# Performance work log

Hardware: AMD Instinct MI355X
Metric: run time of the kernel (lower is better)

Reference implementation:

```python
import jax, jax.numpy as jnp
import numpy as np
import math

DIM = 256

def setup_inputs() -> dict:
    key = jax.random.key(0)
    kx, kq, kk, kv = jax.random.split(key, 4)
    B, N, D = 2, 8192, DIM
    x = jax.random.normal(kx, (B, N, D), dtype=jnp.float32)
    s = 1.0 / math.sqrt(D)  # ~ PyTorch Linear init scale
    Wq = jax.random.uniform(kq, (D, D), dtype=jnp.float32, minval=-s, maxval=s)
    Wk = jax.random.uniform(kk, (D, D), dtype=jnp.float32, minval=-s, maxval=s)
    Wv = jax.random.uniform(kv, (D, D), dtype=jnp.float32, minval=-s, maxval=s)
    return {"x": x, "Wq": Wq, "Wk": Wk, "Wv": Wv}

def reference(x, Wq, Wk, Wv):
    # x: [B, N, D]; torch Linear computes x @ W.T
    Q = jnp.einsum('bnd,ed->bne', x, Wq)
    K = jnp.einsum('bnd,ed->bne', x, Wk)
    V = jnp.einsum('bnd,ed->bne', x, Wv)
    D = x.shape[-1]
    scores = jnp.einsum('bqd,bkd->bqk', Q, K) / jnp.sqrt(jnp.float32(D))
    # NOTE: softmax over dim=1 (the query axis), matching the original code
    attn = jax.nn.softmax(scores, axis=1)  # [B, N, N]
    out = jnp.einsum('bqk,bkd->bqd', attn, V)
    return out
```

## Files before the change

kernel.cpp:

```cpp
#include <hip/hip_runtime.h>
#include <hip/hip_bf16.h>


#define N_ 8192
#define SCALE 0.0625f

typedef __attribute__((ext_vector_type(8))) short short8;
typedef __attribute__((ext_vector_type(4))) float f32x4;
typedef __attribute__((ext_vector_type(4))) unsigned short ushort4_t;

__device__ inline unsigned short f2bf(float f) {
    unsigned int x = __float_as_uint(f);
    unsigned int r = (x + 0x7fffu + ((x >> 16) & 1u)) >> 16;
    return (unsigned short)r;
}

__device__ inline short8 ldg8(const unsigned short* p) {
    return *reinterpret_cast<const short8*>(p);
}

__device__ inline short8 cvt8(const float* p) {
    float4 a = *(const float4*)p;
    float4 b = *(const float4*)(p + 4);
    short8 r;
    r[0] = (short)f2bf(a.x); r[1] = (short)f2bf(a.y);
    r[2] = (short)f2bf(a.z); r[3] = (short)f2bf(a.w);
    r[4] = (short)f2bf(b.x); r[5] = (short)f2bf(b.y);
    r[6] = (short)f2bf(b.z); r[7] = (short)f2bf(b.w);
    return r;
}

__device__ inline f32x4 mfma16(short8 a, short8 b, f32x4 c) {
    return __builtin_amdgcn_mfma_f32_16x16x32_bf16(a, b, c, 0, 0, 0);
}

__device__ inline float bf2f(unsigned short u) {
    return __uint_as_float(((unsigned)u) << 16);
}

#define PIN8(v) asm volatile("" : "+v"(v))

typedef __attribute__((address_space(3))) unsigned int lds_u32;
typedef __attribute__((address_space(1))) const unsigned int glb_u32;
__device__ __forceinline__ void gll16(const void* g, void* l) {
    __builtin_amdgcn_global_load_lds((glb_u32*)g, (lds_u32*)l, 16, 0, 0);
}
#define WAIT_VM0()   asm volatile("s_waitcnt vmcnt(0)" ::: "memory")
#define WAIT_LGKM0() asm volatile("s_waitcnt lgkmcnt(0)" ::: "memory")
#define BARRIER()    __builtin_amdgcn_s_barrier()

__global__ __launch_bounds__(256) void k_cvtw(
    const float* __restrict__ Wq, const float* __restrict__ Wk,
    const float* __restrict__ Wv, unsigned short* __restrict__ Wb)
{
    int t = blockIdx.x * 256 + threadIdx.x;
    int e8 = t * 8;
    const float* src = (e8 < 65536) ? Wq + e8
                     : (e8 < 131072) ? Wk + (e8 - 65536)
                                     : Wv + (e8 - 131072);
    *reinterpret_cast<short8*>(Wb + e8) = cvt8(src);
}

__global__ __launch_bounds__(512) void k_proj(
    const float* __restrict__ x, const unsigned short* __restrict__ Wb,
    unsigned short* __restrict__ Qb, unsigned short* __restrict__ Kb,
    unsigned short* __restrict__ Vt)
{
    __shared__ unsigned short sX[64 * 256];
    int rb = blockIdx.x;
    int tid = threadIdx.x, w = tid >> 6, lane = tid & 63;
    int lr = lane & 15, lg = lane >> 4;

#pragma unroll
    for (int i = 0; i < 4; ++i) {
        int g = tid + i * 512;
        int r = g >> 5, c = g & 31;
        int off = (r * 512 + c * 16) ^ ((r & 7) << 4);
        *reinterpret_cast<short8*>(reinterpret_cast<char*>(sX) + off) =
            cvt8(x + (size_t)(rb * 64 + r) * 256 + c * 8);
    }
    __syncthreads();

    f32x4 acc[4][6] = {};
#pragma unroll
    for (int ks = 0; ks < 8; ++ks) {
        int coff = (ks * 32 + lg * 8) * 2;
        short8 xf[4];
#pragma unroll
        for (int rf = 0; rf < 4; ++rf) {
            int row = rf * 16 + lr;
            int off = (row * 512 + coff) ^ ((row & 7) << 4);
            xf[rf] = *reinterpret_cast<const short8*>(
                reinterpret_cast<const char*>(sX) + off);
        }
#pragma unroll
        for (int cf = 0; cf < 6; ++cf) {
            int e = w * 96 + cf * 16 + lr;
            short8 bfr = ldg8(Wb + (size_t)e * 256 + ks * 32 + lg * 8);
#pragma unroll
            for (int rf = 0; rf < 4; ++rf)
                acc[rf][cf] = mfma16(xf[rf], bfr, acc[rf][cf]);
        }
    }

#pragma unroll
    for (int rf = 0; rf < 4; ++rf)
#pragma unroll
        for (int cf = 0; cf < 6; ++cf) {
            int e0c = w * 96 + cf * 16;
            int mat = e0c >> 8;
            int ecol = (e0c & 255) + lr;
            int rbase = rb * 64 + rf * 16 + lg * 4;
            if (mat < 2) {
                unsigned short* dst = (mat == 0) ? Qb : Kb;
#pragma unroll
                for (int r = 0; r < 4; ++r)
                    dst[(size_t)(rbase + r) * 256 + ecol] = f2bf(acc[rf][cf][r]);
            } else {
                int bidx = rbase >> 13, nr = rbase & 8191;
                ushort4_t v;
#pragma unroll
                for (int r = 0; r < 4; ++r) v[r] = f2bf(acc[rf][cf][r]);
                *reinterpret_cast<ushort4_t*>(
                    Vt + ((size_t)bidx * 256 + ecol) * 8192 + nr) = v;
            }
        }
}

__global__ __launch_bounds__(512, 1) void k_zv(
    const unsigned short* __restrict__ Qb, const unsigned short* __restrict__ Kb,
    unsigned short* __restrict__ Vt)
{
    extern __shared__ char smem[];
    __shared__ float zred[8][32];
    __shared__ float zfin[64];
    const int kt = blockIdx.x, b = blockIdx.y;
    const int tid = threadIdx.x, w = tid >> 6, lane = tid & 63;
    const int lr = lane & 15, lg = lane >> 4;
    const int qs = w & 3, kh = w >> 2;

    short8 kfr[2][8];
#pragma unroll
    for (int kn = 0; kn < 2; ++kn)
#pragma unroll
        for (int ks = 0; ks < 8; ++ks) {
            kfr[kn][ks] = ldg8(
                Kb + (size_t)(b * N_ + kt * 64 + kh * 32 + kn * 16 + lr) * 256
                   + ks * 32 + lg * 8);
            PIN8(kfr[kn][ks]);
        }

    int eoff[8], doff[8];
#pragma unroll
    for (int i = 0; i < 8; ++i) {
        int L = i * 512 + w * 64 + lane;
        int r = L >> 5, c = (L & 31) ^ (r & 7);
        eoff[i] = r * 256 + c * 8;
        doff[i] = L * 16;
    }
    const unsigned short* qbase = Qb + (size_t)b * N_ * 256;

#pragma unroll
    for (int i = 0; i < 8; ++i)
        gll16(qbase + eoff[i], smem + doff[i]);

    float zs0 = 0.f, zs1 = 0.f;
    for (int it = 0; it < 64; ++it) {
        const int cur = it & 1;
        const char* sQ = smem + cur * 65536;

        WAIT_VM0();
        BARRIER();
        __builtin_amdgcn_sched_barrier(0);

        if (it + 1 < 64) {
            const unsigned short* qsrc = qbase + (size_t)(it + 1) * 128 * 256;
            char* nQ = smem + (cur ^ 1) * 65536;
#pragma unroll
            for (int i = 0; i < 8; ++i)
                gll16(qsrc + eoff[i], nQ + doff[i]);
        }

        f32x4 acc[2][2] = {};
        __builtin_amdgcn_s_setprio(1);
#pragma unroll
        for (int ks = 0; ks < 8; ++ks) {
            int coff = (ks * 32 + lg * 8) * 2;
#pragma unroll
            for (int qf = 0; qf < 2; ++qf) {
                int row = qs * 32 + qf * 16 + lr;
                int off = (row * 512 + coff) ^ ((row & 7) << 4);
                short8 qa = *reinterpret_cast<const short8*>(sQ + off);
                acc[qf][0] = mfma16(qa, kfr[0][ks], acc[qf][0]);
                acc[qf][1] = mfma16(qa, kfr[1][ks], acc[qf][1]);
            }
        }
        __builtin_amdgcn_s_setprio(0);

#pragma unroll
        for (int qf = 0; qf < 2; ++qf)
#pragma unroll
            for (int r = 0; r < 4; ++r) {
                zs0 += __expf(acc[qf][0][r] * SCALE);
                zs1 += __expf(acc[qf][1][r] * SCALE);
            }
    }

    zs0 += __shfl_xor(zs0, 16); zs0 += __shfl_xor(zs0, 32);
    zs1 += __shfl_xor(zs1, 16); zs1 += __shfl_xor(zs1, 32);
    if (lg == 0) {
        zred[w][lr]      = zs0;
        zred[w][16 + lr] = zs1;
    }
    __syncthreads();
    if (tid < 64) {
        int kh2 = tid >> 5, kc = tid & 31;
        float z = zred[kh2 * 4 + 0][kc] + zred[kh2 * 4 + 1][kc] +
                  zred[kh2 * 4 + 2][kc] + zred[kh2 * 4 + 3][kc];
        zfin[tid] = 1.0f / z;
    }
    __syncthreads();

#pragma unroll
    for (int i = 0; i < 4; ++i) {
        int G = i * 512 + tid;
        int d = G >> 3, c = G & 7;
        unsigned short* p =
            Vt + ((size_t)b * 256 + d) * 8192 + kt * 64 + c * 8;
        short8 v = *reinterpret_cast<short8*>(p);
        short8 o;
#pragma unroll
        for (int j = 0; j < 8; ++j)
            o[j] = (short)f2bf(bf2f((unsigned short)v[j]) * zfin[c * 8 + j]);
        *reinterpret_cast<short8*>(p) = o;
    }
}

__global__ __launch_bounds__(512, 1) void k_attn(
    const unsigned short* __restrict__ Qb, const unsigned short* __restrict__ Kb,
    const unsigned short* __restrict__ Vt, float* __restrict__ out)
{
    extern __shared__ char smem[];
    const int qt = blockIdx.x, b = blockIdx.y;
    const int tid = threadIdx.x, w = tid >> 6, lane = tid & 63;
    const int lr = lane & 15, lg = lane >> 4;
    const int qbase = qt * 64;
    const int wqs = w >> 2;
    const int wks = w & 3;
    const int wds = w & 3;
    const int q0 = wqs * 32;

    const unsigned short* srcK[4];
    const unsigned short* srcV[4];
#pragma unroll
    for (int i = 0; i < 4; ++i) {
        int L = w * 256 + i * 64 + lane;
        int r = L >> 5, c = (L & 31) ^ (r & 7);
        srcK[i] = Kb + (size_t)(b * N_ + r) * 256 + c * 8;
        int d = L >> 3, c2 = (L & 7) ^ (d & 7);
        srcV[i] = Vt + ((size_t)b * 256 + d) * 8192 + c2 * 8;
    }

#pragma unroll
    for (int i = 0; i < 4; ++i) {
        gll16(srcK[i], smem + (size_t)(w * 256 + i * 64) * 16);
        gll16(srcV[i], smem + 65536 + (size_t)(w * 256 + i * 64) * 16);
        srcK[i] += 64 * 256;
        srcV[i] += 64;
    }

    short8 qfr[2][8];
#pragma unroll
    for (int qf = 0; qf < 2; ++qf) {
        const unsigned short* qrow =
            Qb + (size_t)(b * N_ + qbase + q0 + qf * 16 + lr) * 256;
#pragma unroll
        for (int ks = 0; ks < 8; ++ks) {
            qfr[qf][ks] = ldg8(qrow + ks * 32 + lg * 8);
            PIN8(qfr[qf][ks]);
        }
    }

    f32x4 acco[2][4] = {};

    for (int kt = 0; kt < 128; ++kt) {
        const int cur = kt & 1;
        char* sK = smem + cur * 32768;
        char* sV = smem + 65536 + cur * 32768;
        char* sP = smem + 131072;

        WAIT_VM0();
        BARRIER();
        __builtin_amdgcn_sched_barrier(0);

        if (kt + 1 < 128) {
            char* nK = smem + (cur ^ 1) * 32768;
            char* nV = smem + 65536 + (cur ^ 1) * 32768;
#pragma unroll
            for (int i = 0; i < 4; ++i) {
                gll16(srcK[i], nK + (size_t)(w * 256 + i * 64) * 16);
                gll16(srcV[i], nV + (size_t)(w * 256 + i * 64) * 16);
                srcK[i] += 64 * 256;
                srcV[i] += 64;
            }
        }

        f32x4 sacc[2] = {};
        __builtin_amdgcn_s_setprio(1);
#pragma unroll
        for (int ks = 0; ks < 8; ++ks) {
            int krow = wks * 16 + lr;
            int coff = (ks * 32 + lg * 8) * 2;
            int off = (krow * 512 + coff) ^ ((krow & 7) << 4);
            short8 kb = *reinterpret_cast<const short8*>(sK + off);
            sacc[0] = mfma16(qfr[0][ks], kb, sacc[0]);
            sacc[1] = mfma16(qfr[1][ks], kb, sacc[1]);
        }
        __builtin_amdgcn_s_setprio(0);

#pragma unroll
        for (int qf = 0; qf < 2; ++qf)
#pragma unroll
            for (int r = 0; r < 4; ++r) {
                float p = __expf(sacc[qf][r] * SCALE);
                int q = q0 + qf * 16 + lg * 4 + r;
                int kcol = wks * 16 + lr;
                int off = (q * 128 + kcol * 2) ^ ((q & 7) << 4);
                *reinterpret_cast<unsigned short*>(sP + off) = f2bf(p);
            }

        WAIT_LGKM0();
        BARRIER();
        __builtin_amdgcn_sched_barrier(0);

        __builtin_amdgcn_s_setprio(1);
#pragma unroll
        for (int kk = 0; kk < 2; ++kk) {
            int coff = (kk * 32 + lg * 8) * 2;
            short8 pa[2];
#pragma unroll
            for (int qf = 0; qf < 2; ++qf) {
                int qq = q0 + qf * 16 + lr;
                int offa = (qq * 128 + coff) ^ ((qq & 7) << 4);
                pa[qf] = *reinterpret_cast<const short8*>(sP + offa);
            }
#pragma unroll
            for (int df = 0; df < 4; ++df) {
                int d = wds * 64 + df * 16 + lr;
                int offb = (d * 128 + coff) ^ ((d & 7) << 4);
                short8 vb = *reinterpret_cast<const short8*>(sV + offb);
                acco[0][df] = mfma16(pa[0], vb, acco[0][df]);
                acco[1][df] = mfma16(pa[1], vb, acco[1][df]);
            }
        }
        __builtin_amdgcn_s_setprio(0);
    }

#pragma unroll
    for (int qf = 0; qf < 2; ++qf)
#pragma unroll
        for (int df = 0; df < 4; ++df) {
            int d = wds * 64 + df * 16 + lr;
            int q0r = qbase + q0 + qf * 16 + lg * 4;
#pragma unroll
            for (int r = 0; r < 4; ++r)
                out[(size_t)(b * N_ + q0r + r) * 256 + d] = acco[qf][df][r];
        }
}

extern "C" void kernel_launch(void* const* d_in, const int* in_sizes, int n_in,
                              void* d_out, int out_size, void* d_ws, size_t ws_size,
                              hipStream_t stream)
{
    const float* x  = (const float*)d_in[0];
    const float* Wq = (const float*)d_in[1];
    const float* Wk = (const float*)d_in[2];
    const float* Wv = (const float*)d_in[3];

    char* ws = (char*)d_ws;
    unsigned short* Qb = (unsigned short*)(ws);
    unsigned short* Kb = (unsigned short*)(ws + 8388608);
    unsigned short* Vt = (unsigned short*)(ws + 16777216);
    unsigned short* Wb = (unsigned short*)(ws + 25165824);
    float* out = (float*)d_out;

    k_cvtw<<<dim3(96), dim3(256), 0, stream>>>(Wq, Wk, Wv, Wb);
    k_proj<<<dim3(256), dim3(512), 0, stream>>>(x, Wb, Qb, Kb, Vt);

    hipFuncSetAttribute((const void*)k_zv,
                        hipFuncAttributeMaxDynamicSharedMemorySize, 131072);
    k_zv<<<dim3(128, 2), dim3(512), 131072, stream>>>(Qb, Kb, Vt);

    hipFuncSetAttribute((const void*)k_attn,
                        hipFuncAttributeMaxDynamicSharedMemorySize, 139264);
    k_attn<<<dim3(128, 2), dim3(512), 139264, stream>>>(Qb, Kb, Vt, out);
}
```

Baseline: 303.9 us.

## Software-pipeline PV matmul one tile behind QK and load V fragments directly

The attention loop now computes the P·V product for the previous key tile in the same phase as the current Q·K product, with P double-buffered in shared memory so one barrier per iteration is removed. V is no longer staged through LDS; each lane loads its V fragments straight from global memory into registers, which shrinks dynamic shared memory from about 136KB to 80KB. The trade-off is uncached global V loads per wave (redundant across waves sharing d-columns) and possible latency exposure, since the loads are issued right before use, plus a tail epilogue for the last tile.

After: 449.4 us. 1.48x slower.

```diff
diff --git a/kernel.cpp b/kernel.cpp
--- a/kernel.cpp
+++ b/kernel.cpp
@@ -251,23 +251,23 @@
     const int q0 = wqs * 32;
 
     const unsigned short* srcK[4];
-    const unsigned short* srcV[4];
 #pragma unroll
     for (int i = 0; i < 4; ++i) {
         int L = w * 256 + i * 64 + lane;
         int r = L >> 5, c = (L & 31) ^ (r & 7);
         srcK[i] = Kb + (size_t)(b * N_ + r) * 256 + c * 8;
-        int d = L >> 3, c2 = (L & 7) ^ (d & 7);
-        srcV[i] = Vt + ((size_t)b * 256 + d) * 8192 + c2 * 8;
-    }
-
+    }
 #pragma unroll
     for (int i = 0; i < 4; ++i) {
         gll16(srcK[i], smem + (size_t)(w * 256 + i * 64) * 16);
-        gll16(srcV[i], smem + 65536 + (size_t)(w * 256 + i * 64) * 16);
         srcK[i] += 64 * 256;
-        srcV[i] += 64;
-    }
+    }
+
+    const unsigned short* vrow[4];
+#pragma unroll
+    for (int df = 0; df < 4; ++df)
+        vrow[df] = Vt + ((size_t)(b * 256 + wds * 64 + df * 16 + lr)) * 8192
+                      + lg * 8;
 
     short8 qfr[2][8];
 #pragma unroll
@@ -285,23 +285,31 @@
 
     for (int kt = 0; kt < 128; ++kt) {
         const int cur = kt & 1;
-        char* sK = smem + cur * 32768;
-        char* sV = smem + 65536 + cur * 32768;
-        char* sP = smem + 131072;
+        char* sK  = smem + cur * 32768;
+        char* sPw = smem + 65536 + cur * 8192;
+        const char* sPr = smem + 65536 + (cur ^ 1) * 8192;
 
         WAIT_VM0();
+        WAIT_LGKM0();
         BARRIER();
         __builtin_amdgcn_sched_barrier(0);
 
         if (kt + 1 < 128) {
             char* nK = smem + (cur ^ 1) * 32768;
-            char* nV = smem + 65536 + (cur ^ 1) * 32768;
 #pragma unroll
             for (int i = 0; i < 4; ++i) {
                 gll16(srcK[i], nK + (size_t)(w * 256 + i * 64) * 16);
-                gll16(srcV[i], nV + (size_t)(w * 256 + i * 64) * 16);
                 srcK[i] += 64 * 256;
-                srcV[i] += 64;
+            }
+        }
+
+        short8 vfr[8];
+        if (kt > 0) {
+            int kg = (kt - 1) * 64;
+#pragma unroll
+            for (int df = 0; df < 4; ++df) {
+                vfr[df * 2 + 0] = ldg8(vrow[df] + kg);
+                vfr[df * 2 + 1] = ldg8(vrow[df] + kg + 32);
             }
         }
 
@@ -316,6 +324,24 @@
             sacc[0] = mfma16(qfr[0][ks], kb, sacc[0]);
             sacc[1] = mfma16(qfr[1][ks], kb, sacc[1]);
         }
+        if (kt > 0) {
+#pragma unroll
+            for (int kk = 0; kk < 2; ++kk) {
+                int coff = (kk * 32 + lg * 8) * 2;
+                short8 pa[2];
+#pragma unroll
+                for (int qf = 0; qf < 2; ++qf) {
+                    int qq = q0 + qf * 16 + lr;
+                    int offa = (qq * 128 + coff) ^ ((qq & 7) << 4);
+                    pa[qf] = *reinterpret_cast<const short8*>(sPr + offa);
+                }
+#pragma unroll
+                for (int df = 0; df < 4; ++df) {
+                    acco[0][df] = mfma16(pa[0], vfr[df * 2 + kk], acco[0][df]);
+                    acco[1][df] = mfma16(pa[1], vfr[df * 2 + kk], acco[1][df]);
+                }
+            }
+        }
         __builtin_amdgcn_s_setprio(0);
 
 #pragma unroll
@@ -326,14 +352,21 @@
                 int q = q0 + qf * 16 + lg * 4 + r;
                 int kcol = wks * 16 + lr;
                 int off = (q * 128 + kcol * 2) ^ ((q & 7) << 4);
-                *reinterpret_cast<unsigned short*>(sP + off) = f2bf(p);
-            }
-
-        WAIT_LGKM0();
-        BARRIER();
-        __builtin_amdgcn_sched_barrier(0);
-
-        __builtin_amdgcn_s_setprio(1);
+                *reinterpret_cast<unsigned short*>(sPw + off) = f2bf(p);
+            }
+    }
+
+    WAIT_LGKM0();
+    BARRIER();
+    {
+        const char* sPr = smem + 65536 + (127 & 1) * 8192;
+        int kg = 127 * 64;
+        short8 vfr[8];
+#pragma unroll
+        for (int df = 0; df < 4; ++df) {
+            vfr[df * 2 + 0] = ldg8(vrow[df] + kg);
+            vfr[df * 2 + 1] = ldg8(vrow[df] + kg + 32);
+        }
 #pragma unroll
         for (int kk = 0; kk < 2; ++kk) {
             int coff = (kk * 32 + lg * 8) * 2;
@@ -342,18 +375,14 @@
             for (int qf = 0; qf < 2; ++qf) {
                 int qq = q0 + qf * 16 + lr;
                 int offa = (qq * 128 + coff) ^ ((qq & 7) << 4);
-                pa[qf] = *reinterpret_cast<const short8*>(sP + offa);
+                pa[qf] = *reinterpret_cast<const short8*>(sPr + offa);
             }
 #pragma unroll
             for (int df = 0; df < 4; ++df) {
-                int d = wds * 64 + df * 16 + lr;
-                int offb = (d * 128 + coff) ^ ((d & 7) << 4);
-                short8 vb = *reinterpret_cast<const short8*>(sV + offb);
-                acco[0][df] = mfma16(pa[0], vb, acco[0][df]);
-                acco[1][df] = mfma16(pa[1], vb, acco[1][df]);
-            }
-        }
-        __builtin_amdgcn_s_setprio(0);
+                acco[0][df] = mfma16(pa[0], vfr[df * 2 + kk], acco[0][df]);
+                acco[1][df] = mfma16(pa[1], vfr[df * 2 + kk], acco[1][df]);
+            }
+        }
     }
 
 #pragma unroll
@@ -392,6 +421,6 @@
     k_zv<<<dim3(128, 2), dim3(512), 131072, stream>>>(Qb, Kb, Vt);
 
     hipFuncSetAttribute((const void*)k_attn,
-                        hipFuncAttributeMaxDynamicSharedMemorySize, 139264);
-    k_attn<<<dim3(128, 2), dim3(512), 139264, stream>>>(Qb, Kb, Vt, out);
-}
+                        hipFuncAttributeMaxDynamicSharedMemorySize, 81920);
+    k_attn<<<dim3(128, 2), dim3(512), 81920, stream>>>(Qb, Kb, Vt, out);
+}
```

## Software-pipeline QK and PV stages, load V fragments directly to registers

Applied to the files above, without the earlier changes.

Restructures the attention loop so the PV product for tile t-1 runs in the same phase as the QK product for tile t, using double-buffered P in shared memory, which removes one barrier per iteration. V fragments are now loaded straight from global memory into registers, one tile ahead, instead of being staged through LDS. This cuts LDS usage from 139264 to 81920 bytes. The cost is more registers and uncoalesced-ish per-lane global V loads whose latency must hide behind a single iteration.

After: 425.3 us. +39.9%, slower.

```diff
diff --git a/kernel.cpp b/kernel.cpp
--- a/kernel.cpp
+++ b/kernel.cpp
@@ -251,23 +251,23 @@
     const int q0 = wqs * 32;
 
     const unsigned short* srcK[4];
-    const unsigned short* srcV[4];
 #pragma unroll
     for (int i = 0; i < 4; ++i) {
         int L = w * 256 + i * 64 + lane;
         int r = L >> 5, c = (L & 31) ^ (r & 7);
         srcK[i] = Kb + (size_t)(b * N_ + r) * 256 + c * 8;
-        int d = L >> 3, c2 = (L & 7) ^ (d & 7);
-        srcV[i] = Vt + ((size_t)b * 256 + d) * 8192 + c2 * 8;
-    }
-
+    }
 #pragma unroll
     for (int i = 0; i < 4; ++i) {
         gll16(srcK[i], smem + (size_t)(w * 256 + i * 64) * 16);
-        gll16(srcV[i], smem + 65536 + (size_t)(w * 256 + i * 64) * 16);
         srcK[i] += 64 * 256;
-        srcV[i] += 64;
-    }
+    }
+
+    const unsigned short* vrow[4];
+#pragma unroll
+    for (int df = 0; df < 4; ++df)
+        vrow[df] = Vt + ((size_t)(b * 256 + wds * 64 + df * 16 + lr)) * 8192
+                      + lg * 8;
 
     short8 qfr[2][8];
 #pragma unroll
@@ -282,78 +282,105 @@
     }
 
     f32x4 acco[2][4] = {};
-
-    for (int kt = 0; kt < 128; ++kt) {
-        const int cur = kt & 1;
-        char* sK = smem + cur * 32768;
-        char* sV = smem + 65536 + cur * 32768;
-        char* sP = smem + 131072;
-
-        WAIT_VM0();
-        BARRIER();
-        __builtin_amdgcn_sched_barrier(0);
-
-        if (kt + 1 < 128) {
-            char* nK = smem + (cur ^ 1) * 32768;
-            char* nV = smem + 65536 + (cur ^ 1) * 32768;
-#pragma unroll
-            for (int i = 0; i < 4; ++i) {
-                gll16(srcK[i], nK + (size_t)(w * 256 + i * 64) * 16);
-                gll16(srcV[i], nV + (size_t)(w * 256 + i * 64) * 16);
-                srcK[i] += 64 * 256;
-                srcV[i] += 64;
-            }
-        }
-
-        f32x4 sacc[2] = {};
-        __builtin_amdgcn_s_setprio(1);
-#pragma unroll
-        for (int ks = 0; ks < 8; ++ks) {
-            int krow = wks * 16 + lr;
-            int coff = (ks * 32 + lg * 8) * 2;
-            int off = (krow * 512 + coff) ^ ((krow & 7) << 4);
-            short8 kb = *reinterpret_cast<const short8*>(sK + off);
-            sacc[0] = mfma16(qfr[0][ks], kb, sacc[0]);
-            sacc[1] = mfma16(qfr[1][ks], kb, sacc[1]);
-        }
-        __builtin_amdgcn_s_setprio(0);
-
-#pragma unroll
-        for (int qf = 0; qf < 2; ++qf)
-#pragma unroll
-            for (int r = 0; r < 4; ++r) {
-                float p = __expf(sacc[qf][r] * SCALE);
-                int q = q0 + qf * 16 + lg * 4 + r;
-                int kcol = wks * 16 + lr;
-                int off = (q * 128 + kcol * 2) ^ ((q & 7) << 4);
-                *reinterpret_cast<unsigned short*>(sP + off) = f2bf(p);
-            }
-
-        WAIT_LGKM0();
-        BARRIER();
-        __builtin_amdgcn_sched_barrier(0);
-
-        __builtin_amdgcn_s_setprio(1);
+    short8 vfA[8], vfB[8];
+    int kg = 0;
+
+#define AITER(CUR, VLOAD, VCONS, DO_STAGE, DO_PV)                             \
+    do {                                                                      \
+        WAIT_VM0();                                                           \
+        WAIT_LGKM0();                                                         \
+        BARRIER();                                                            \
+        __builtin_amdgcn_sched_barrier(0);                                    \
+        char* sK  = smem + (CUR) * 32768;                                     \
+        char* sPw = smem + 65536 + (CUR) * 8192;                              \
+        const char* sPr = smem + 65536 + ((CUR) ^ 1) * 8192;                  \
+        if (DO_STAGE) {                                                       \
+            char* nK = smem + ((CUR) ^ 1) * 32768;                            \
+            _Pragma("unroll") for (int i = 0; i < 4; ++i) {                   \
+                gll16(srcK[i], nK + (size_t)(w * 256 + i * 64) * 16);         \
+                srcK[i] += 64 * 256;                                          \
+            }                                                                 \
+        }                                                                     \
+        _Pragma("unroll") for (int df = 0; df < 4; ++df) {                    \
+            VLOAD[df * 2 + 0] = ldg8(vrow[df] + kg);                          \
+            VLOAD[df * 2 + 1] = ldg8(vrow[df] + kg + 32);                     \
+        }                                                                     \
+        kg += 64;                                                             \
+        f32x4 sacc[2] = {};                                                   \
+        __builtin_amdgcn_s_setprio(1);                                        \
+        _Pragma("unroll") for (int ks = 0; ks < 8; ++ks) {                    \
+            int krow = wks * 16 + lr;                                         \
+            int coff = (ks * 32 + lg * 8) * 2;                                \
+            int off = (krow * 512 + coff) ^ ((krow & 7) << 4);                \
+            short8 kb = *reinterpret_cast<const short8*>(sK + off);           \
+            sacc[0] = mfma16(qfr[0][ks], kb, sacc[0]);                        \
+            sacc[1] = mfma16(qfr[1][ks], kb, sacc[1]);                        \
+        }                                                                     \
+        if (DO_PV) {                                                          \
+            _Pragma("unroll") for (int kk = 0; kk < 2; ++kk) {                \
+                int coff = (kk * 32 + lg * 8) * 2;                            \
+                short8 pa0, pa1;                                              \
+                {                                                             \
+                    int qq = q0 + lr;                                         \
+                    int offa = (qq * 128 + coff) ^ ((qq & 7) << 4);           \
+                    pa0 = *reinterpret_cast<const short8*>(sPr + offa);       \
+                }                                                             \
+                {                                                             \
+                    int qq = q0 + 16 + lr;                                    \
+                    int offa = (qq * 128 + coff) ^ ((qq & 7) << 4);           \
+                    pa1 = *reinterpret_cast<const short8*>(sPr + offa);       \
+                }                                                             \
+                _Pragma("unroll") for (int df = 0; df < 4; ++df) {            \
+                    acco[0][df] = mfma16(pa0, VCONS[df * 2 + kk], acco[0][df]); \
+                    acco[1][df] = mfma16(pa1, VCONS[df * 2 + kk], acco[1][df]); \
+                }                                                             \
+            }                                                                 \
+        }                                                                     \
+        __builtin_amdgcn_s_setprio(0);                                        \
+        _Pragma("unroll") for (int qf = 0; qf < 2; ++qf)                      \
+            _Pragma("unroll") for (int r = 0; r < 4; ++r) {                   \
+                float p = __expf(sacc[qf][r] * SCALE);                        \
+                int q = q0 + qf * 16 + lg * 4 + r;                            \
+                int kcol = wks * 16 + lr;                                     \
+                int off = (q * 128 + kcol * 2) ^ ((q & 7) << 4);              \
+                *reinterpret_cast<unsigned short*>(sPw + off) = f2bf(p);      \
+            }                                                                 \
+    } while (0)
+
+    AITER(0, vfA, vfB, true, false);
+#pragma unroll 1
+    for (int t2 = 0; t2 < 63; ++t2) {
+        AITER(1, vfB, vfA, true, true);
+        AITER(0, vfA, vfB, true, true);
+    }
+    AITER(1, vfB, vfA, false, true);
+#undef AITER
+
+    WAIT_VM0();
+    WAIT_LGKM0();
+    BARRIER();
+    {
+        const char* sPr = smem + 65536 + 1 * 8192;
 #pragma unroll
         for (int kk = 0; kk < 2; ++kk) {
             int coff = (kk * 32 + lg * 8) * 2;
-            short8 pa[2];
-#pragma unroll
-            for (int qf = 0; qf < 2; ++qf) {
-                int qq = q0 + qf * 16 + lr;
+            short8 pa0, pa1;
+            {
+                int qq = q0 + lr;
                 int offa = (qq * 128 + coff) ^ ((qq & 7) << 4);
-                pa[qf] = *reinterpret_cast<const short8*>(sP + offa);
+                pa0 = *reinterpret_cast<const short8*>(sPr + offa);
+            }
+            {
+                int qq = q0 + 16 + lr;
+                int offa = (qq * 128 + coff) ^ ((qq & 7) << 4);
+                pa1 = *reinterpret_cast<const short8*>(sPr + offa);
             }
 #pragma unroll
             for (int df = 0; df < 4; ++df) {
-                int d = wds * 64 + df * 16 + lr;
-                int offb = (d * 128 + coff) ^ ((d & 7) << 4);
-                short8 vb = *reinterpret_cast<const short8*>(sV + offb);
-                acco[0][df] = mfma16(pa[0], vb, acco[0][df]);
-                acco[1][df] = mfma16(pa[1], vb, acco[1][df]);
-            }
-        }
-        __builtin_amdgcn_s_setprio(0);
+                acco[0][df] = mfma16(pa0, vfB[df * 2 + kk], acco[0][df]);
+                acco[1][df] = mfma16(pa1, vfB[df * 2 + kk], acco[1][df]);
+            }
+        }
     }
 
 #pragma unroll
@@ -392,6 +419,6 @@
     k_zv<<<dim3(128, 2), dim3(512), 131072, stream>>>(Qb, Kb, Vt);
 
     hipFuncSetAttribute((const void*)k_attn,
-                        hipFuncAttributeMaxDynamicSharedMemorySize, 139264);
-    k_attn<<<dim3(128, 2), dim3(512), 139264, stream>>>(Qb, Kb, Vt, out);
-}
+                        hipFuncAttributeMaxDynamicSharedMemorySize, 81920);
+    k_attn<<<dim3(128, 2), dim3(512), 81920, stream>>>(Qb, Kb, Vt, out);
+}
```

## Stage projection weights through double-buffered LDS with async global-to-LDS loads

Applied to the files above, without the earlier changes.

The projection kernel now keeps each wave's X fragments in registers and streams the bf16 weight matrix in 64-row chunks into a double-buffered LDS region using global_load_lds. The next chunk loads while the current one feeds the MFMAs. This replaces per-wave direct global loads of weight fragments, which were re-read redundantly across waves. The cost is 96KB of dynamic LDS, a single block per CU, a barrier per chunk, and smaller per-chunk accumulator tiles.

New measurement: 300.8 us. About the same (-1.0%).

```diff
diff --git a/kernel.cpp b/kernel.cpp
--- a/kernel.cpp
+++ b/kernel.cpp
@@ -61,15 +61,32 @@
     *reinterpret_cast<short8*>(Wb + e8) = cvt8(src);
 }
 
-__global__ __launch_bounds__(512) void k_proj(
+__global__ __launch_bounds__(512, 1) void k_proj(
     const float* __restrict__ x, const unsigned short* __restrict__ Wb,
     unsigned short* __restrict__ Qb, unsigned short* __restrict__ Kb,
     unsigned short* __restrict__ Vt)
 {
-    __shared__ unsigned short sX[64 * 256];
-    int rb = blockIdx.x;
-    int tid = threadIdx.x, w = tid >> 6, lane = tid & 63;
-    int lr = lane & 15, lg = lane >> 4;
+    extern __shared__ char smem[];
+    unsigned short* sX = (unsigned short*)smem;
+    char* sW = smem + 32768;
+    const int rb = blockIdx.x;
+    const int tid = threadIdx.x, w = tid >> 6, lane = tid & 63;
+    const int lr = lane & 15, lg = lane >> 4;
+    const int wqs = w >> 2, wes = w & 3;
+
+    int eoff[4], doff[4];
+#pragma unroll
+    for (int i = 0; i < 4; ++i) {
+        int L = tid + i * 512;
+        int r = L >> 5, c = (L & 31) ^ (r & 7);
+        eoff[i] = r * 256 + c * 8;
+        doff[i] = L * 16;
+    }
+
+    const unsigned short* wsrc = Wb;
+#pragma unroll
+    for (int i = 0; i < 4; ++i)
+        gll16(wsrc + eoff[i], sW + doff[i]);
 
 #pragma unroll
     for (int i = 0; i < 4; ++i) {
@@ -81,50 +98,64 @@
     }
     __syncthreads();
 
-    f32x4 acc[4][6] = {};
-#pragma unroll
-    for (int ks = 0; ks < 8; ++ks) {
-        int coff = (ks * 32 + lg * 8) * 2;
-        short8 xf[4];
-#pragma unroll
-        for (int rf = 0; rf < 4; ++rf) {
-            int row = rf * 16 + lr;
-            int off = (row * 512 + coff) ^ ((row & 7) << 4);
-            xf[rf] = *reinterpret_cast<const short8*>(
+    short8 xf[2][8];
+#pragma unroll
+    for (int qf = 0; qf < 2; ++qf)
+#pragma unroll
+        for (int ks = 0; ks < 8; ++ks) {
+            int row = wqs * 32 + qf * 16 + lr;
+            int off = (row * 512 + (ks * 32 + lg * 8) * 2) ^ ((row & 7) << 4);
+            xf[qf][ks] = *reinterpret_cast<const short8*>(
                 reinterpret_cast<const char*>(sX) + off);
-        }
-#pragma unroll
-        for (int cf = 0; cf < 6; ++cf) {
-            int e = w * 96 + cf * 16 + lr;
-            short8 bfr = ldg8(Wb + (size_t)e * 256 + ks * 32 + lg * 8);
-#pragma unroll
-            for (int rf = 0; rf < 4; ++rf)
-                acc[rf][cf] = mfma16(xf[rf], bfr, acc[rf][cf]);
-        }
-    }
-
-#pragma unroll
-    for (int rf = 0; rf < 4; ++rf)
-#pragma unroll
-        for (int cf = 0; cf < 6; ++cf) {
-            int e0c = w * 96 + cf * 16;
-            int mat = e0c >> 8;
-            int ecol = (e0c & 255) + lr;
-            int rbase = rb * 64 + rf * 16 + lg * 4;
+            PIN8(xf[qf][ks]);
+        }
+
+    for (int c = 0; c < 12; ++c) {
+        const int cur = c & 1;
+        const char* sWc = sW + cur * 32768;
+
+        WAIT_VM0();
+        BARRIER();
+        __builtin_amdgcn_sched_barrier(0);
+
+        if (c + 1 < 12) {
+            const unsigned short* wn = Wb + (size_t)(c + 1) * 64 * 256;
+            char* nW = sW + (cur ^ 1) * 32768;
+#pragma unroll
+            for (int i = 0; i < 4; ++i)
+                gll16(wn + eoff[i], nW + doff[i]);
+        }
+
+        f32x4 acc[2] = {};
+#pragma unroll
+        for (int ks = 0; ks < 8; ++ks) {
+            int row = wes * 16 + lr;
+            int off = (row * 512 + (ks * 32 + lg * 8) * 2) ^ ((row & 7) << 4);
+            short8 wf = *reinterpret_cast<const short8*>(sWc + off);
+            acc[0] = mfma16(xf[0][ks], wf, acc[0]);
+            acc[1] = mfma16(xf[1][ks], wf, acc[1]);
+        }
+
+        int mat = c >> 2;
+        int ecol = (c & 3) * 64 + wes * 16 + lr;
+#pragma unroll
+        for (int qf = 0; qf < 2; ++qf) {
+            int rbase = rb * 64 + wqs * 32 + qf * 16 + lg * 4;
             if (mat < 2) {
                 unsigned short* dst = (mat == 0) ? Qb : Kb;
 #pragma unroll
                 for (int r = 0; r < 4; ++r)
-                    dst[(size_t)(rbase + r) * 256 + ecol] = f2bf(acc[rf][cf][r]);
+                    dst[(size_t)(rbase + r) * 256 + ecol] = f2bf(acc[qf][r]);
             } else {
                 int bidx = rbase >> 13, nr = rbase & 8191;
                 ushort4_t v;
 #pragma unroll
-                for (int r = 0; r < 4; ++r) v[r] = f2bf(acc[rf][cf][r]);
+                for (int r = 0; r < 4; ++r) v[r] = f2bf(acc[qf][r]);
                 *reinterpret_cast<ushort4_t*>(
                     Vt + ((size_t)bidx * 256 + ecol) * 8192 + nr) = v;
             }
         }
+    }
 }
 
 __global__ __launch_bounds__(512, 1) void k_zv(
@@ -385,7 +416,10 @@
     float* out = (float*)d_out;
 
     k_cvtw<<<dim3(96), dim3(256), 0, stream>>>(Wq, Wk, Wv, Wb);
-    k_proj<<<dim3(256), dim3(512), 0, stream>>>(x, Wb, Qb, Kb, Vt);
+
+    hipFuncSetAttribute((const void*)k_proj,
+                        hipFuncAttributeMaxDynamicSharedMemorySize, 98304);
+    k_proj<<<dim3(256), dim3(512), 98304, stream>>>(x, Wb, Qb, Kb, Vt);
 
     hipFuncSetAttribute((const void*)k_zv,
                         hipFuncAttributeMaxDynamicSharedMemorySize, 131072);
```
